# Kernel optimization log

Hardware: AMD Instinct MI355X
Metric: run time of the kernel (lower is better)

Reference implementation:

```python
import jax, jax.numpy as jnp
import numpy as np

B, H, S, D = 4, 16, 2048, 64
MASK_FILL = 1e-12  # module quirk: masked scores set to 1e-12, not -inf


def setup_inputs() -> dict:
    key = jax.random.key(0)
    kq, kk, kv, km = jax.random.split(key, 4)
    q = jax.random.normal(kq, (B, H, S, D), dtype=jnp.float32)
    k = jax.random.normal(kk, (B, H, S, D), dtype=jnp.float32)
    v = jax.random.normal(kv, (B, H, S, D), dtype=jnp.float32)
    mask = jax.random.randint(km, (B, 1, 1, S), 0, 2, dtype=jnp.int32)
    return {"q": q, "k": k, "v": v, "mask": mask}


def reference(q, k, v, mask):
    dim = k.shape[-1]
    # scores: [B,H,S,S]
    scores = jnp.einsum('bhid,bhjd->bhij', q, k) * (dim ** -0.5)
    # faithful to masked_fill(mask == 0, 1e-12)
    scores = jnp.where(mask == 0, jnp.asarray(MASK_FILL, scores.dtype), scores)
    attention = jax.nn.softmax(scores, axis=-1)
    output = jnp.einsum('bhij,bhjd->bhid', attention, v)
    return output, attention
```

## Files before the change

### kernel.cpp

```cpp
#include <hip/hip_runtime.h>
#include <hip/hip_bf16.h>

namespace {

constexpr int S = 2048;
constexpr int D = 64;
constexpr float QSCALE = 0.125f * 1.4426950408889634f;

typedef __bf16 bf16x8 __attribute__((ext_vector_type(8)));
typedef float f32x16 __attribute__((ext_vector_type(16)));
typedef unsigned int uint32x4 __attribute__((ext_vector_type(4)));

#if __has_builtin(__builtin_amdgcn_exp2f)
__device__ __forceinline__ float fexp2(float x) { return __builtin_amdgcn_exp2f(x); }
#else
__device__ __forceinline__ float fexp2(float x) { return exp2f(x); }
#endif

__device__ __forceinline__ bf16x8 cvt8s(float4 a, float4 b, float s) {
    bf16x8 f;
    f[0] = (__bf16)(a.x * s); f[1] = (__bf16)(a.y * s);
    f[2] = (__bf16)(a.z * s); f[3] = (__bf16)(a.w * s);
    f[4] = (__bf16)(b.x * s); f[5] = (__bf16)(b.y * s);
    f[6] = (__bf16)(b.z * s); f[7] = (__bf16)(b.w * s);
    return f;
}
__device__ __forceinline__ bf16x8 cvt8(float4 a, float4 b) {
    bf16x8 f;
    f[0] = (__bf16)a.x; f[1] = (__bf16)a.y;
    f[2] = (__bf16)a.z; f[3] = (__bf16)a.w;
    f[4] = (__bf16)b.x; f[5] = (__bf16)b.y;
    f[6] = (__bf16)b.z; f[7] = (__bf16)b.w;
    return f;
}

}

__global__ void __launch_bounds__(256)
attn_fused(const float* __restrict__ qg, const float* __restrict__ kg,
           const float* __restrict__ vg, const int* __restrict__ mg,
           float* __restrict__ og, float* __restrict__ ag)
{
    __shared__ bf16x8 kstage[2][256];
    __shared__ alignas(16) unsigned short plds_all[4][32][40];

    const int tid  = threadIdx.x;
    const int lane = tid & 63;
    const int w    = tid >> 6;
    const int l31  = lane & 31;
    const int h2   = lane >> 5;

    const int wid = (blockIdx.x & 7) * 128 + (blockIdx.x >> 3);
    const int bh  = wid >> 4;
    const int q0  = ((wid & 15) * 4 + w) * 32;
    const int b   = bh >> 4;

    const float* qrow = qg + ((size_t)bh * S + q0 + l31) * D + 8 * h2;
    const float* vb_  = vg + (size_t)bh * S * D;
    const int*   mrow = mg + b * S + l31;
    float* att  = ag + (size_t)bh * S * S + (size_t)q0 * S;
    float* orow = og + ((size_t)bh * S + q0) * D;
    unsigned short (*plds)[40] = plds_all[w];

    const int srow  = tid >> 3;
    const int scol  = tid & 7;
    const int sslot = srow * 8 + (scol ^ (srow & 7));
    const float* ksrc = kg + (size_t)bh * S * D + (size_t)srow * D + scol * 8;

    int kslot[4];
#pragma unroll
    for (int t = 0; t < 4; ++t)
        kslot[t] = l31 * 8 + ((2 * t + h2) ^ (l31 & 7));

    bf16x8 qa[4];
#pragma unroll
    for (int t = 0; t < 4; ++t) {
        const float4* p4 = (const float4*)(qrow + 16 * t);
        qa[t] = cvt8s(p4[0], p4[1], QSCALE);
    }

    unsigned long long mbits = 0ull;
#pragma unroll 8
    for (int t = 0; t < 64; ++t)
        mbits |= (unsigned long long)(mrow[t * 32] != 0) << t;

    {
        const float4* p4 = (const float4*)ksrc;
        kstage[0][sslot] = cvt8(p4[0], p4[1]);
    }
    __syncthreads();

    float sums[16];
#pragma unroll
    for (int r = 0; r < 16; ++r) sums[r] = 0.f;

    int cur = 0;
    for (int j0 = 0; j0 < S; j0 += 32) {
        const bool more = (j0 + 32) < S;
        float4 na{}, nb{};
        if (more) {
            const float4* p4 = (const float4*)(ksrc + (size_t)(j0 + 32) * D);
            na = p4[0]; nb = p4[1];
        }
        f32x16 acc;
#pragma unroll
        for (int r = 0; r < 16; ++r) acc[r] = 0.f;
#pragma unroll
        for (int t = 0; t < 4; ++t)
            acc = __builtin_amdgcn_mfma_f32_32x32x16_bf16(qa[t], kstage[cur][kslot[t]], acc, 0, 0, 0);
        const bool mf = (mbits >> (j0 >> 5)) & 1;
#pragma unroll
        for (int r = 0; r < 16; ++r)
            sums[r] += mf ? fexp2(acc[r]) : 1.0f;
        if (more) kstage[cur ^ 1][sslot] = cvt8(na, nb);
        __syncthreads();
        cur ^= 1;
    }
#pragma unroll
    for (int r = 0; r < 16; ++r) {
        float s = sums[r];
        s += __shfl_xor(s, 1);
        s += __shfl_xor(s, 2);
        s += __shfl_xor(s, 4);
        s += __shfl_xor(s, 8);
        s += __shfl_xor(s, 16);
        sums[r] = 1.0f / s;
    }

    {
        const float4* p4 = (const float4*)ksrc;
        kstage[0][sslot] = cvt8(p4[0], p4[1]);
    }
    __syncthreads();

    f32x16 oacc[2];
#pragma unroll
    for (int g = 0; g < 2; ++g)
#pragma unroll
        for (int r = 0; r < 16; ++r) oacc[g][r] = 0.f;

    cur = 0;
    for (int j0 = 0; j0 < S; j0 += 32) {
        const bool more = (j0 + 32) < S;
        float4 na{}, nb{};
        if (more) {
            const float4* p4 = (const float4*)(ksrc + (size_t)(j0 + 32) * D);
            na = p4[0]; nb = p4[1];
        }
        bf16x8 vfr[2][2];
#pragma unroll
        for (int f = 0; f < 2; ++f) {
            const float* vrow = vb_ + (size_t)(j0 + 16 * f + 8 * h2) * D + l31;
#pragma unroll
            for (int g = 0; g < 2; ++g) {
                bf16x8 vf;
#pragma unroll
                for (int e = 0; e < 8; ++e)
                    vf[e] = (__bf16)vrow[e * D + 32 * g];
                vfr[f][g] = vf;
            }
        }
        f32x16 acc;
#pragma unroll
        for (int r = 0; r < 16; ++r) acc[r] = 0.f;
#pragma unroll
        for (int t = 0; t < 4; ++t)
            acc = __builtin_amdgcn_mfma_f32_32x32x16_bf16(qa[t], kstage[cur][kslot[t]], acc, 0, 0, 0);
        const bool mf = (mbits >> (j0 >> 5)) & 1;
#pragma unroll
        for (int r = 0; r < 16; ++r) {
            float p = mf ? fexp2(acc[r]) : 1.0f;
            p *= sums[r];
            const int qr = (r & 3) + 8 * (r >> 2) + 4 * h2;
            __builtin_nontemporal_store(p, &att[(size_t)qr * S + j0 + l31]);
            plds[qr][l31] = __builtin_bit_cast(unsigned short, (__bf16)p);
        }
#pragma unroll
        for (int f = 0; f < 2; ++f) {
            uint32x4 u;
            __builtin_memcpy(&u, &plds[l31][16 * f + 8 * h2], 16);
            bf16x8 pa = __builtin_bit_cast(bf16x8, u);
#pragma unroll
            for (int g = 0; g < 2; ++g)
                oacc[g] = __builtin_amdgcn_mfma_f32_32x32x16_bf16(pa, vfr[f][g], oacc[g], 0, 0, 0);
        }
        if (more) kstage[cur ^ 1][sslot] = cvt8(na, nb);
        __syncthreads();
        cur ^= 1;
    }

#pragma unroll
    for (int g = 0; g < 2; ++g)
#pragma unroll
        for (int r = 0; r < 16; ++r) {
            const int qr = (r & 3) + 8 * (r >> 2) + 4 * h2;
            __builtin_nontemporal_store(oacc[g][r], &orow[(size_t)qr * D + 32 * g + l31]);
        }
}

extern "C" void kernel_launch(void* const* d_in, const int* in_sizes, int n_in,
                              void* d_out, int out_size, void* d_ws, size_t ws_size,
                              hipStream_t stream) {
    const float* q    = (const float*)d_in[0];
    const float* k    = (const float*)d_in[1];
    const float* v    = (const float*)d_in[2];
    const int*   mask = (const int*)d_in[3];
    float* out = (float*)d_out;
    float* att = out + (size_t)64 * S * D;
    dim3 grid(1024), block(256);
    hipLaunchKernelGGL(attn_fused, grid, block, 0, stream,
                       q, k, v, mask, out, att);
}
```

Baseline: 315.6 us.

## Move PV accumulation into first pass with transposed QK and shared V staging

Computes the unnormalized P·V product during the first (row-sum) pass by using a transposed QK^T MFMA so that P fragments can be formed in registers via permlane32 swaps instead of an LDS round-trip. The output is then scaled by the inverse row sum. V is staged cooperatively into swizzled shared memory with double buffering instead of per-lane strided global loads. The second pass only recomputes scores and writes the attention matrix. It also adds a packed mask in LDS, s_setprio around the MFMAs, and a launch-bounds occupancy hint. The cost is extra LDS use and some register pressure, and accumulating unnormalized bf16 P risks some precision loss.

```diff
diff --git a/kernel.cpp b/kernel.cpp
--- a/kernel.cpp
+++ b/kernel.cpp
@@ -9,7 +9,6 @@
 
 typedef __bf16 bf16x8 __attribute__((ext_vector_type(8)));
 typedef float f32x16 __attribute__((ext_vector_type(16)));
-typedef unsigned int uint32x4 __attribute__((ext_vector_type(4)));
 
 #if __has_builtin(__builtin_amdgcn_exp2f)
 __device__ __forceinline__ float fexp2(float x) { return __builtin_amdgcn_exp2f(x); }
@@ -33,16 +32,22 @@
     f[6] = (__bf16)b.z; f[7] = (__bf16)b.w;
     return f;
 }
-
-}
-
-__global__ void __launch_bounds__(256)
+__device__ __forceinline__ unsigned int pkbf(float lo, float hi) {
+    unsigned int a = (unsigned int)__builtin_bit_cast(unsigned short, (__bf16)lo);
+    unsigned int b = (unsigned int)__builtin_bit_cast(unsigned short, (__bf16)hi);
+    return a | (b << 16);
+}
+
+}
+
+__global__ void __launch_bounds__(256, 4)
 attn_fused(const float* __restrict__ qg, const float* __restrict__ kg,
            const float* __restrict__ vg, const int* __restrict__ mg,
            float* __restrict__ og, float* __restrict__ ag)
 {
     __shared__ bf16x8 kstage[2][256];
-    __shared__ alignas(16) unsigned short plds_all[4][32][40];
+    __shared__ bf16x8 vstage[2][256];
+    __shared__ unsigned int mlds[64];
 
     const int tid  = threadIdx.x;
     const int lane = tid & 63;
@@ -57,20 +62,30 @@
 
     const float* qrow = qg + ((size_t)bh * S + q0 + l31) * D + 8 * h2;
     const float* vb_  = vg + (size_t)bh * S * D;
-    const int*   mrow = mg + b * S + l31;
     float* att  = ag + (size_t)bh * S * S + (size_t)q0 * S;
     float* orow = og + ((size_t)bh * S + q0) * D;
-    unsigned short (*plds)[40] = plds_all[w];
 
     const int srow  = tid >> 3;
     const int scol  = tid & 7;
     const int sslot = srow * 8 + (scol ^ (srow & 7));
     const float* ksrc = kg + (size_t)bh * S * D + (size_t)srow * D + scol * 8;
-
     int kslot[4];
 #pragma unroll
     for (int t = 0; t < 4; ++t)
         kslot[t] = l31 * 8 + ((2 * t + h2) ^ (l31 & 7));
+
+    const int vd = tid & 63;
+    const int vw = tid >> 6;
+    const int vwslot = vd * 4 + (vw ^ ((vd >> 1) & 3));
+    const float* vsrc = vb_ + vd;
+    int vslot[2][2];
+#pragma unroll
+    for (int f = 0; f < 2; ++f)
+#pragma unroll
+        for (int g = 0; g < 2; ++g) {
+            const int d = l31 + 32 * g;
+            vslot[f][g] = d * 4 + ((2 * f + h2) ^ ((d >> 1) & 3));
+        }
 
     bf16x8 qa[4];
 #pragma unroll
@@ -79,53 +94,119 @@
         qa[t] = cvt8s(p4[0], p4[1], QSCALE);
     }
 
-    unsigned long long mbits = 0ull;
-#pragma unroll 8
-    for (int t = 0; t < 64; ++t)
-        mbits |= (unsigned long long)(mrow[t * 32] != 0) << t;
+    if (tid < 64) {
+        const int4* mp = (const int4*)(mg + (size_t)b * S + 32 * tid);
+        unsigned int bits = 0;
+#pragma unroll
+        for (int k = 0; k < 8; ++k) {
+            int4 m = mp[k];
+            bits |= (unsigned int)(m.x != 0) << (4 * k);
+            bits |= (unsigned int)(m.y != 0) << (4 * k + 1);
+            bits |= (unsigned int)(m.z != 0) << (4 * k + 2);
+            bits |= (unsigned int)(m.w != 0) << (4 * k + 3);
+        }
+        mlds[tid] = bits;
+    }
 
     {
         const float4* p4 = (const float4*)ksrc;
         kstage[0][sslot] = cvt8(p4[0], p4[1]);
+        bf16x8 vv;
+#pragma unroll
+        for (int k = 0; k < 8; ++k)
+            vv[k] = (__bf16)vsrc[(size_t)(8 * vw + k) * D];
+        vstage[0][vwslot] = vv;
     }
     __syncthreads();
 
-    float sums[16];
-#pragma unroll
-    for (int r = 0; r < 16; ++r) sums[r] = 0.f;
+    float ssum = 0.f;
+    f32x16 oacc[2];
+#pragma unroll
+    for (int g = 0; g < 2; ++g)
+#pragma unroll
+        for (int r = 0; r < 16; ++r) oacc[g][r] = 0.f;
 
     int cur = 0;
     for (int j0 = 0; j0 < S; j0 += 32) {
         const bool more = (j0 + 32) < S;
-        float4 na{}, nb{};
+        float4 kna{}, knb{};
+        float vp[8];
         if (more) {
             const float4* p4 = (const float4*)(ksrc + (size_t)(j0 + 32) * D);
-            na = p4[0]; nb = p4[1];
-        }
+            kna = p4[0]; knb = p4[1];
+#pragma unroll
+            for (int k = 0; k < 8; ++k)
+                vp[k] = vsrc[(size_t)(j0 + 32 + 8 * vw + k) * D];
+        }
+        const unsigned int mw = mlds[j0 >> 5];
+
         f32x16 acc;
 #pragma unroll
         for (int r = 0; r < 16; ++r) acc[r] = 0.f;
+        __builtin_amdgcn_s_setprio(1);
 #pragma unroll
         for (int t = 0; t < 4; ++t)
-            acc = __builtin_amdgcn_mfma_f32_32x32x16_bf16(qa[t], kstage[cur][kslot[t]], acc, 0, 0, 0);
-        const bool mf = (mbits >> (j0 >> 5)) & 1;
-#pragma unroll
-        for (int r = 0; r < 16; ++r)
-            sums[r] += mf ? fexp2(acc[r]) : 1.0f;
-        if (more) kstage[cur ^ 1][sslot] = cvt8(na, nb);
+            acc = __builtin_amdgcn_mfma_f32_32x32x16_bf16(kstage[cur][kslot[t]], qa[t], acc, 0, 0, 0);
+        __builtin_amdgcn_s_setprio(0);
+
+        const unsigned int mq = mw >> (4 * h2);
+        unsigned int pk[8];
+#pragma unroll
+        for (int qd = 0; qd < 4; ++qd) {
+            float pv[4];
+#pragma unroll
+            for (int i = 0; i < 4; ++i) {
+                const float e = fexp2(acc[4 * qd + i]);
+                pv[i] = ((mq >> (i + 8 * qd)) & 1) ? e : 1.0f;
+                ssum += pv[i];
+            }
+            pk[2 * qd]     = pkbf(pv[0], pv[1]);
+            pk[2 * qd + 1] = pkbf(pv[2], pv[3]);
+        }
+        asm volatile("v_permlane32_swap_b32 %0, %1" : "+v"(pk[0]), "+v"(pk[2]));
+        asm volatile("v_permlane32_swap_b32 %0, %1" : "+v"(pk[1]), "+v"(pk[3]));
+        asm volatile("v_permlane32_swap_b32 %0, %1" : "+v"(pk[4]), "+v"(pk[6]));
+        asm volatile("v_permlane32_swap_b32 %0, %1" : "+v"(pk[5]), "+v"(pk[7]));
+        typedef unsigned int uint4v __attribute__((ext_vector_type(4)));
+        uint4v u0 = {pk[0], pk[1], pk[2], pk[3]};
+        uint4v u1 = {pk[4], pk[5], pk[6], pk[7]};
+        bf16x8 pa[2];
+        pa[0] = __builtin_bit_cast(bf16x8, u0);
+        pa[1] = __builtin_bit_cast(bf16x8, u1);
+
+        __builtin_amdgcn_s_setprio(1);
+#pragma unroll
+        for (int f = 0; f < 2; ++f)
+#pragma unroll
+            for (int g = 0; g < 2; ++g)
+                oacc[g] = __builtin_amdgcn_mfma_f32_32x32x16_bf16(pa[f], vstage[cur][vslot[f][g]], oacc[g], 0, 0, 0);
+        __builtin_amdgcn_s_setprio(0);
+
+        if (more) {
+            kstage[cur ^ 1][sslot] = cvt8(kna, knb);
+            bf16x8 vv;
+#pragma unroll
+            for (int k = 0; k < 8; ++k) vv[k] = (__bf16)vp[k];
+            vstage[cur ^ 1][vwslot] = vv;
+        }
         __syncthreads();
         cur ^= 1;
     }
-#pragma unroll
-    for (int r = 0; r < 16; ++r) {
-        float s = sums[r];
-        s += __shfl_xor(s, 1);
-        s += __shfl_xor(s, 2);
-        s += __shfl_xor(s, 4);
-        s += __shfl_xor(s, 8);
-        s += __shfl_xor(s, 16);
-        sums[r] = 1.0f / s;
-    }
+
+    const float inv = 1.0f / (ssum + __shfl_xor(ssum, 32));
+    float invq[16];
+#pragma unroll
+    for (int r = 0; r < 16; ++r)
+        invq[r] = __shfl(inv, (r & 3) + 8 * (r >> 2) + 4 * h2);
+
+#pragma unroll
+    for (int g = 0; g < 2; ++g)
+#pragma unroll
+        for (int r = 0; r < 16; ++r) {
+            const int qr = (r & 3) + 8 * (r >> 2) + 4 * h2;
+            __builtin_nontemporal_store(oacc[g][r] * invq[r],
+                                        &orow[(size_t)qr * D + 32 * g + l31]);
+        }
 
     {
         const float4* p4 = (const float4*)ksrc;
@@ -133,69 +214,36 @@
     }
     __syncthreads();
 
-    f32x16 oacc[2];
-#pragma unroll
-    for (int g = 0; g < 2; ++g)
-#pragma unroll
-        for (int r = 0; r < 16; ++r) oacc[g][r] = 0.f;
-
     cur = 0;
     for (int j0 = 0; j0 < S; j0 += 32) {
         const bool more = (j0 + 32) < S;
-        float4 na{}, nb{};
+        float4 kna{}, knb{};
         if (more) {
             const float4* p4 = (const float4*)(ksrc + (size_t)(j0 + 32) * D);
-            na = p4[0]; nb = p4[1];
-        }
-        bf16x8 vfr[2][2];
-#pragma unroll
-        for (int f = 0; f < 2; ++f) {
-            const float* vrow = vb_ + (size_t)(j0 + 16 * f + 8 * h2) * D + l31;
-#pragma unroll
-            for (int g = 0; g < 2; ++g) {
-                bf16x8 vf;
-#pragma unroll
-                for (int e = 0; e < 8; ++e)
-                    vf[e] = (__bf16)vrow[e * D + 32 * g];
-                vfr[f][g] = vf;
-            }
-        }
+            kna = p4[0]; knb = p4[1];
+        }
+        const bool mf = (mlds[j0 >> 5] >> l31) & 1;
+
         f32x16 acc;
 #pragma unroll
         for (int r = 0; r < 16; ++r) acc[r] = 0.f;
+        __builtin_amdgcn_s_setprio(1);
 #pragma unroll
         for (int t = 0; t < 4; ++t)
             acc = __builtin_amdgcn_mfma_f32_32x32x16_bf16(qa[t], kstage[cur][kslot[t]], acc, 0, 0, 0);
-        const bool mf = (mbits >> (j0 >> 5)) & 1;
+        __builtin_amdgcn_s_setprio(0);
+
 #pragma unroll
         for (int r = 0; r < 16; ++r) {
             float p = mf ? fexp2(acc[r]) : 1.0f;
-            p *= sums[r];
+            p *= invq[r];
             const int qr = (r & 3) + 8 * (r >> 2) + 4 * h2;
             __builtin_nontemporal_store(p, &att[(size_t)qr * S + j0 + l31]);
-            plds[qr][l31] = __builtin_bit_cast(unsigned short, (__bf16)p);
-        }
-#pragma unroll
-        for (int f = 0; f < 2; ++f) {
-            uint32x4 u;
-            __builtin_memcpy(&u, &plds[l31][16 * f + 8 * h2], 16);
-            bf16x8 pa = __builtin_bit_cast(bf16x8, u);
-#pragma unroll
-            for (int g = 0; g < 2; ++g)
-                oacc[g] = __builtin_amdgcn_mfma_f32_32x32x16_bf16(pa, vfr[f][g], oacc[g], 0, 0, 0);
-        }
-        if (more) kstage[cur ^ 1][sslot] = cvt8(na, nb);
+        }
+        if (more) kstage[cur ^ 1][sslot] = cvt8(kna, knb);
         __syncthreads();
         cur ^= 1;
     }
-
-#pragma unroll
-    for (int g = 0; g < 2; ++g)
-#pragma unroll
-        for (int r = 0; r < 16; ++r) {
-            const int qr = (r & 3) + 8 * (r >> 2) + 4 * h2;
-            __builtin_nontemporal_store(oacc[g][r], &orow[(size_t)qr * D + 32 * g + l31]);
-        }
 }
 
 extern "C" void kernel_launch(void* const* d_in, const int* in_sizes, int n_in,
```

Result: faster. 291.9 us (-7.5%).
